# Performance work log

Hardware: AMD Instinct MI355X
Metric: run time of the kernel (lower is better)

## Reference

```python
import jax, jax.numpy as jnp
import numpy as np

N_NODES = 100000
N_EDGES = 800000
N_GRAPHS = 512
D_IN = 128
D_H = 128
N_LAYERS = 3
EPS = 1e-5


def setup_inputs() -> dict:
    key = jax.random.key(0)
    ks = jax.random.split(key, 8)
    x = jax.random.normal(ks[0], (N_NODES, D_IN), dtype=jnp.float32)
    edge_index = jax.random.randint(ks[1], (2, N_EDGES), 0, N_NODES, dtype=jnp.int64)
    batch = jnp.sort(jax.random.randint(ks[2], (N_NODES,), 0, N_GRAPHS, dtype=jnp.int64))
    s = 1.0 / np.sqrt(D_H)
    Ws = jax.random.normal(ks[3], (N_LAYERS, D_H, D_H), dtype=jnp.float32) * s
    bs = jnp.zeros((N_LAYERS, D_H), dtype=jnp.float32)
    gammas = jnp.ones((N_LAYERS, D_H), dtype=jnp.float32)
    betas = jnp.zeros((N_LAYERS, D_H), dtype=jnp.float32)
    W1 = jax.random.normal(ks[4], (D_H, D_H), dtype=jnp.float32) * s
    b1 = jnp.zeros((D_H,), dtype=jnp.float32)
    W2 = jax.random.normal(ks[5], (D_H, 1), dtype=jnp.float32) * s
    b2 = jnp.zeros((1,), dtype=jnp.float32)
    return {"x": x, "edge_index": edge_index, "batch": batch, "Ws": Ws, "bs": bs,
            "gammas": gammas, "betas": betas, "W1": W1, "b1": b1, "W2": W2, "b2": b2}


def reference(x, edge_index, batch, Ws, bs, gammas, betas, W1, b1, W2, b2):
    N = x.shape[0]
    src, dst = edge_index[0], edge_index[1]
    # GCN symmetric norm with self-loops: deg = in-degree + 1 (self loop weight 1)
    deg = jax.ops.segment_sum(jnp.ones_like(dst, dtype=jnp.float32), dst, num_segments=N) + 1.0
    dinv = jax.lax.rsqrt(deg)                      # [N]
    enorm = (dinv[src] * dinv[dst])[:, None]       # [E,1]
    self_w = (1.0 / deg)[:, None]                  # [N,1] self-loop norm dinv_i^2

    h = x
    for l in range(N_LAYERS):
        h = h @ Ws[l]                                                    # linear first (as PyG GCNConv)
        h = jax.ops.segment_sum(enorm * h[src], dst, num_segments=N) + h * self_w
        h = h + bs[l]
        # BatchNorm1d, training-mode per-feature stats (biased variance)
        mu = jnp.mean(h, axis=0)
        var = jnp.mean(jnp.square(h - mu), axis=0)
        h = (h - mu) * jax.lax.rsqrt(var + EPS) * gammas[l] + betas[l]
        h = jax.nn.relu(h)                                               # dropout p=0 -> identity

    # global mean pool over subgraphs
    sums = jax.ops.segment_sum(h, batch, num_segments=N_GRAPHS)
    cnt = jax.ops.segment_sum(jnp.ones((N,), jnp.float32), batch, num_segments=N_GRAPHS)
    Z = sums / jnp.maximum(cnt, 1.0)[:, None]

    # MLP head
    hz = jax.nn.relu(Z @ W1 + b1)
    logits = hz @ W2 + b2                           # [N_GRAPHS, 1]
    return logits
```

## Files before the change

kernel.cpp:

```cpp
#include <hip/hip_runtime.h>
#include <hip/hip_bf16.h>
#include <hip/hip_fp16.h>

#define N_NODES 100000
#define N_EDGES 800000
#define N_GRAPHS 512
#define D 128
#define EPSV 1e-5f

#define NBLK 256
#define EPB  3125
#define NBUK 391
#define MAXB 3072

#define LSTR 68
#define WOFF 4352

#define NSLOT 128

typedef _Float16 half8 __attribute__((ext_vector_type(8)));
typedef float floatx16 __attribute__((ext_vector_type(16)));

__device__ __forceinline__ float relu_f(float x){ return fmaxf(x, 0.0f); }

__device__ __forceinline__ void scan512(int* sd, int t)
{
    for (int off = 1; off < 512; off <<= 1){
        int i2 = t + 256;
        int v1 = (t  >= off) ? sd[t  - off] : 0;
        int v2 = (i2 >= off) ? sd[i2 - off] : 0;
        __syncthreads();
        sd[t]  += v1;
        sd[i2] += v2;
        __syncthreads();
    }
}

__global__ __launch_bounds__(256) void k_front(const int* __restrict__ dst,
                                               int* __restrict__ blockHist,
                                               const float* __restrict__ Ws,
                                               unsigned int* __restrict__ wpack,
                                               unsigned int* __restrict__ zbase,
                                               int zn,
                                               const int* __restrict__ batch,
                                               int* __restrict__ gstart,
                                               int* __restrict__ row_ptr)
{
    __shared__ int h[NBUK];
    int j = blockIdx.x, t = threadIdx.x;
    if (j < NBLK){
        for (int u = t; u < NBUK; u += 256) h[u] = 0;
        __syncthreads();
        int e0 = j * EPB;
        for (int e = e0 + t; e < e0 + EPB; e += 256)
            atomicAdd(&h[dst[e] >> 8], 1);
        __syncthreads();
        for (int u = t; u < NBUK; u += 256) blockHist[j * NBUK + u] = h[u];
    } else {
        int b = j - NBLK;
        int idx = b * 256 + t;
        if (idx == 0){
            row_ptr[N_NODES] = N_EDGES;
            gstart[N_GRAPHS] = N_NODES;
        }
        if (idx < 3 * 128 * 64){
            int l  = idx >> 13;
            int r  = idx & 8191;
            int c  = r >> 6;
            int k2 = r & 63;
            const float* W = Ws + l * D * D;
            __half2 hh = __floats2half2_rn(W[(size_t)(2 * k2) * D + c],
                                           W[(size_t)(2 * k2 + 1) * D + c]);
            wpack[idx] = *(unsigned int*)&hh;
        }
        int stride = 96 * 256;
        for (int i = idx; i < zn; i += stride) zbase[i] = 0u;
        if (idx < N_GRAPHS){
            int g = idx;
            int lo = 0, hi = N_NODES;
            while (lo < hi){ int m = (lo + hi) >> 1; if (batch[m] < g) lo = m + 1; else hi = m; }
            gstart[g] = lo;
        }
    }
}

__global__ __launch_bounds__(256) void k_p2a(const int* __restrict__ blockHist,
                                             int* __restrict__ colScan,
                                             int* __restrict__ bucketTotal)
{
    __shared__ int sd[256];
    int b = blockIdx.x, t = threadIdx.x;
    int v = blockHist[t * NBUK + b];
    sd[t] = v;
    __syncthreads();
    for (int off = 1; off < 256; off <<= 1){
        int u = (t >= off) ? sd[t - off] : 0;
        __syncthreads();
        sd[t] += u;
        __syncthreads();
    }
    colScan[t * NBUK + b] = sd[t] - v;
    if (t == 255) bucketTotal[b] = sd[255];
}

__global__ __launch_bounds__(256) void k_p3(const int* __restrict__ src,
                                            const int* __restrict__ dst,
                                            const int* __restrict__ colScan,
                                            const int* __restrict__ bucketTotal,
                                            int2* __restrict__ ebuf)
{
    __shared__ int sd[512];
    __shared__ int cur[NBUK];
    int j = blockIdx.x, t = threadIdx.x;
    int i2 = t + 256;
    sd[t]  = (t  < NBUK) ? bucketTotal[t]  : 0;
    sd[i2] = (i2 < NBUK) ? bucketTotal[i2] : 0;
    __syncthreads();
    scan512(sd, t);
    if (t < NBUK)
        cur[t]  = (sd[t]  - bucketTotal[t])  + colScan[j * NBUK + t];
    if (i2 < NBUK)
        cur[i2] = (sd[i2] - bucketTotal[i2]) + colScan[j * NBUK + i2];
    __syncthreads();
    int e0 = j * EPB;
    for (int e = e0 + t; e < e0 + EPB; e += 256){
        int s = src[e], d = dst[e];
        int pos = atomicAdd(&cur[d >> 8], 1);
        int2 v; v.x = s; v.y = d;
        ebuf[pos] = v;
    }
}

__global__ __launch_bounds__(256) void k_p4(const int2* __restrict__ ebuf,
                                            const int* __restrict__ bucketTotal,
                                            int* __restrict__ row_ptr,
                                            int* __restrict__ csr_src,
                                            float* __restrict__ dinv)
{
    __shared__ int2 stash[MAXB];
    __shared__ int sdScan[512];
    __shared__ int bins[256];
    __shared__ int sd[256];
    int b = blockIdx.x, t = threadIdx.x;
    int i2 = t + 256;
    sdScan[t]  = (t  < NBUK) ? bucketTotal[t]  : 0;
    sdScan[i2] = (i2 < NBUK) ? bucketTotal[i2] : 0;
    __syncthreads();
    scan512(sdScan, t);
    int cntb = bucketTotal[b];
    int base = sdScan[b] - cntb;
    bool st = (cntb <= MAXB);
    bins[t] = 0;
    __syncthreads();
    for (int i = t; i < cntb; i += 256){
        int2 ed = ebuf[base + i];
        if (st) stash[i] = ed;
        atomicAdd(&bins[ed.y & 255], 1);
    }
    __syncthreads();
    int a0 = bins[t];
    sd[t] = a0;
    __syncthreads();
    for (int off = 1; off < 256; off <<= 1){
        int v = (t >= off) ? sd[t - off] : 0;
        __syncthreads();
        sd[t] += v;
        __syncthreads();
    }
    int pex = sd[t] - a0;
    int node = b * 256 + t;
    if (node < N_NODES){
        row_ptr[node] = base + pex;
        float d = (float)(a0 + 1);
        dinv[node]  = rsqrtf(d);
    }
    __syncthreads();
    bins[t] = pex;
    __syncthreads();
    for (int i = t; i < cntb; i += 256){
        int2 ed = st ? stash[i] : ebuf[base + i];
        int pos = atomicAdd(&bins[ed.y & 255], 1);
        csr_src[base + pos] = ed.x;
    }
}

__global__ __launch_bounds__(256) void k_gemm(const void* __restrict__ Ain,
                                              const unsigned int* __restrict__ wp,
                                              const float* __restrict__ scale,
                                              const float* __restrict__ shift,
                                              const float* __restrict__ dinv,
                                              __half* __restrict__ outh,
                                              int mode)
{
    __shared__ unsigned int lds32[WOFF + 128 * LSTR];
    int tid = threadIdx.x;
    int rowBase = blockIdx.x * 64;

    if (mode == 0){
        const float* A = (const float*)Ain;
        #pragma unroll
        for (int rep = 0; rep < 8; rep++){
            int f  = rep * 256 + tid;
            int m  = f >> 5;
            int c4 = f & 31;
            int row = rowBase + m;
            if (row >= N_NODES) row = N_NODES - 1;
            float4 v = *(const float4*)(A + (size_t)row * D + c4 * 4);
            __half2 h0 = __floats2half2_rn(v.x, v.y);
            __half2 h1 = __floats2half2_rn(v.z, v.w);
            uint2 u; u.x = *(unsigned int*)&h0; u.y = *(unsigned int*)&h1;
            *(uint2*)&lds32[m * LSTR + 2 * c4] = u;
        }
    } else {
        const __half* A16 = (const __half*)Ain;
        #pragma unroll
        for (int rep = 0; rep < 4; rep++){
            int f  = rep * 256 + tid;
            int m  = f >> 4;
            int c8 = f & 15;
            int row = rowBase + m;
            if (row >= N_NODES) row = N_NODES - 1;
            uint4 v = *(const uint4*)(A16 + (size_t)row * D + c8 * 8);
            float4 sc0 = *(const float4*)(scale + c8 * 8);
            float4 sc1 = *(const float4*)(scale + c8 * 8 + 4);
            float4 sh0 = *(const float4*)(shift + c8 * 8);
            float4 sh1 = *(const float4*)(shift + c8 * 8 + 4);
            float2 f0 = __half22float2(*(__half2*)&v.x);
            float2 f1 = __half22float2(*(__half2*)&v.y);
            float2 f2 = __half22float2(*(__half2*)&v.z);
            float2 f3 = __half22float2(*(__half2*)&v.w);
            f0.x = relu_f(fmaf(f0.x, sc0.x, sh0.x));
            f0.y = relu_f(fmaf(f0.y, sc0.y, sh0.y));
            f1.x = relu_f(fmaf(f1.x, sc0.z, sh0.z));
            f1.y = relu_f(fmaf(f1.y, sc0.w, sh0.w));
            f2.x = relu_f(fmaf(f2.x, sc1.x, sh1.x));
            f2.y = relu_f(fmaf(f2.y, sc1.y, sh1.y));
            f3.x = relu_f(fmaf(f3.x, sc1.z, sh1.z));
            f3.y = relu_f(fmaf(f3.y, sc1.w, sh1.w));
            __half2 h0 = __floats2half2_rn(f0.x, f0.y);
            __half2 h1 = __floats2half2_rn(f1.x, f1.y);
            __half2 h2 = __floats2half2_rn(f2.x, f2.y);
            __half2 h3 = __floats2half2_rn(f3.x, f3.y);
            uint4 u;
            u.x = *(unsigned int*)&h0; u.y = *(unsigned int*)&h1;
            u.z = *(unsigned int*)&h2; u.w = *(unsigned int*)&h3;
            *(uint4*)&lds32[m * LSTR + 4 * c8] = u;
        }
    }
    {
        const uint4* gw = (const uint4*)wp;
        #pragma unroll
        for (int rep = 0; rep < 8; rep++){
            int f = rep * 256 + tid;
            int c = f >> 4;
            int q = f & 15;
            uint4 v = gw[f];
            *(uint4*)&lds32[WOFF + c * LSTR + 4 * q] = v;
        }
    }
    __syncthreads();

    int lane = tid & 63, wv = tid >> 6;
    int quad = lane >> 5;
    int ml   = (lane & 31) + (wv & 1) * 32;
    int cA   = (wv >> 1) * 64;
    int c0   = cA + (lane & 31);
    int c1   = c0 + 32;
    const unsigned int* aRow  = lds32 + ml * LSTR;
    const unsigned int* bRow0 = lds32 + WOFF + c0 * LSTR;
    const unsigned int* bRow1 = lds32 + WOFF + c1 * LSTR;
    floatx16 acc0 = {};
    floatx16 acc1 = {};
    #pragma unroll
    for (int ch = 0; ch < 8; ch++){
        int o = ch * 8 + quad * 4;
        half8 af = *(const half8*)(aRow  + o);
        half8 b0 = *(const half8*)(bRow0 + o);
        half8 b1 = *(const half8*)(bRow1 + o);
        acc0 = __builtin_amdgcn_mfma_f32_32x32x16_f16(af, b0, acc0, 0, 0, 0);
        acc1 = __builtin_amdgcn_mfma_f32_32x32x16_f16(af, b1, acc1, 0, 0, 0);
    }
    int rBase = rowBase + (wv & 1) * 32 + 4 * quad;
    #pragma unroll
    for (int r = 0; r < 16; r++){
        int outRow = rBase + (r & 3) + 8 * (r >> 2);
        if (outRow < N_NODES){
            float dv = dinv[outRow];
            outh[(size_t)outRow * D + c0] = __float2half(acc0[r] * dv);
            outh[(size_t)outRow * D + c1] = __float2half(acc1[r] * dv);
        }
    }
}

__device__ __forceinline__ void accum8(float* acc, uint4 v)
{
    float2 f0 = __half22float2(*(__half2*)&v.x);
    float2 f1 = __half22float2(*(__half2*)&v.y);
    float2 f2 = __half22float2(*(__half2*)&v.z);
    float2 f3 = __half22float2(*(__half2*)&v.w);
    acc[0] += f0.x; acc[1] += f0.y; acc[2] += f1.x; acc[3] += f1.y;
    acc[4] += f2.x; acc[5] += f2.y; acc[6] += f3.x; acc[7] += f3.y;
}

__global__ __launch_bounds__(256) void k_agg(const __half* __restrict__ t,
                                             const int* __restrict__ row_ptr,
                                             const int* __restrict__ csr_src,
                                             const float* __restrict__ dinv,
                                             const float* __restrict__ bias,
                                             __half* __restrict__ outb,
                                             float* __restrict__ Spart,
                                             float* __restrict__ Qpart)
{
    __shared__ float ldsS[4][128];
    __shared__ float ldsQ[4][128];
    int tid  = threadIdx.x;
    int lane = tid & 63;
    int wv   = tid >> 6;
    int q    = lane & 15;
    int g    = lane >> 4;
    const uint4* t4 = (const uint4*)t;
    uint4* out4 = (uint4*)outb;

    float4 bia = ((const float4*)bias)[2 * q];
    float4 bib = ((const float4*)bias)[2 * q + 1];

    float sa[8] = {0.f,0.f,0.f,0.f,0.f,0.f,0.f,0.f};
    float qa[8] = {0.f,0.f,0.f,0.f,0.f,0.f,0.f,0.f};

    int i0 = blockIdx.x * 32 + wv * 8 + g * 2;

    for (int n = 0; n < 2; n++){
        int i  = i0 + n;
        int p  = row_ptr[i];
        int pe = row_ptr[i + 1];
        float acc[8];
        {
            uint4 v = t4[(size_t)i * 16 + q];
            float2 f0 = __half22float2(*(__half2*)&v.x);
            float2 f1 = __half22float2(*(__half2*)&v.y);
            float2 f2 = __half22float2(*(__half2*)&v.z);
            float2 f3 = __half22float2(*(__half2*)&v.w);
            acc[0] = f0.x; acc[1] = f0.y; acc[2] = f1.x; acc[3] = f1.y;
            acc[4] = f2.x; acc[5] = f2.y; acc[6] = f3.x; acc[7] = f3.y;
        }
        for (; p + 4 <= pe; p += 4){
            int s0 = csr_src[p],     s1 = csr_src[p + 1];
            int s2 = csr_src[p + 2], s3 = csr_src[p + 3];
            uint4 v0 = t4[(size_t)s0 * 16 + q];
            uint4 v1 = t4[(size_t)s1 * 16 + q];
            uint4 v2 = t4[(size_t)s2 * 16 + q];
            uint4 v3 = t4[(size_t)s3 * 16 + q];
            accum8(acc, v0); accum8(acc, v1); accum8(acc, v2); accum8(acc, v3);
        }
        for (; p < pe; ++p){
            int s = csr_src[p];
            uint4 v = t4[(size_t)s * 16 + q];
            accum8(acc, v);
        }
        float dvi = dinv[i];
        acc[0] = fmaf(acc[0], dvi, bia.x);
        acc[1] = fmaf(acc[1], dvi, bia.y);
        acc[2] = fmaf(acc[2], dvi, bia.z);
        acc[3] = fmaf(acc[3], dvi, bia.w);
        acc[4] = fmaf(acc[4], dvi, bib.x);
        acc[5] = fmaf(acc[5], dvi, bib.y);
        acc[6] = fmaf(acc[6], dvi, bib.z);
        acc[7] = fmaf(acc[7], dvi, bib.w);
        __half2 o0 = __floats2half2_rn(acc[0], acc[1]);
        __half2 o1 = __floats2half2_rn(acc[2], acc[3]);
        __half2 o2 = __floats2half2_rn(acc[4], acc[5]);
        __half2 o3 = __floats2half2_rn(acc[6], acc[7]);
        uint4 ov;
        ov.x = *(unsigned int*)&o0; ov.y = *(unsigned int*)&o1;
        ov.z = *(unsigned int*)&o2; ov.w = *(unsigned int*)&o3;
        out4[(size_t)i * 16 + q] = ov;
        #pragma unroll
        for (int k = 0; k < 8; k++){
            sa[k] += acc[k];
            qa[k]  = fmaf(acc[k], acc[k], qa[k]);
        }
    }

    #pragma unroll
    for (int k = 0; k < 8; k++){
        sa[k] += __shfl_xor(sa[k], 16);
        sa[k] += __shfl_xor(sa[k], 32);
        qa[k] += __shfl_xor(qa[k], 16);
        qa[k] += __shfl_xor(qa[k], 32);
    }
    if (g == 0){
        #pragma unroll
        for (int k = 0; k < 8; k++){
            ldsS[wv][8 * q + k] = sa[k];
            ldsQ[wv][8 * q + k] = qa[k];
        }
    }
    __syncthreads();
    int slotBase = (blockIdx.x & (NSLOT - 1)) * 128;
    if (tid < 128){
        float s = ldsS[0][tid] + ldsS[1][tid] + ldsS[2][tid] + ldsS[3][tid];
        atomicAdd(&Spart[slotBase + tid], s);
    } else {
        int f = tid - 128;
        float qv = ldsQ[0][f] + ldsQ[1][f] + ldsQ[2][f] + ldsQ[3][f];
        atomicAdd(&Qpart[slotBase + f], qv);
    }
}

__global__ __launch_bounds__(256) void k_fin2(const float* __restrict__ Spart,
                                              const float* __restrict__ Qpart,
                                              const float* __restrict__ gamma,
                                              const float* __restrict__ beta,
                                              float* __restrict__ sc,
                                              float* __restrict__ sh)
{
    int t = threadIdx.x;
    int f = t & 127;
    const float* src = (t < 128) ? Spart : Qpart;
    float acc = 0.f;
    for (int s2 = 0; s2 < NSLOT; s2++)
        acc += src[s2 * 128 + f];
    __shared__ float red[256];
    red[t] = acc;
    __syncthreads();
    if (t < 128){
        float Sv = red[t];
        float Qv = red[t + 128];
        float mean = Sv * (1.0f / N_NODES);
        float var  = fmaxf(Qv * (1.0f / N_NODES) - mean * mean, 0.0f);
        float inv  = rsqrtf(var + EPSV);
        float gm = gamma[f] * inv;
        sc[f] = gm;
        sh[f] = beta[f] - mean * gm;
    }
}

__global__ __launch_bounds__(256) void k_tail(const __half* __restrict__ h,
                                              const int* __restrict__ gstart,
                                              const float* __restrict__ sc,
                                              const float* __restrict__ sh,
                                              const float* __restrict__ W1,
                                              const float* __restrict__ b1,
                                              const float* __restrict__ W2,
                                              const float* __restrict__ b2,
                                              float* __restrict__ out)
{
    __shared__ float part[256];
    __shared__ float z[128];
    __shared__ float red[128];
    int g = blockIdx.x;
    int tid = threadIdx.x;
    int f = tid & 127;
    int hf = tid >> 7;
    int s0 = gstart[g], s1 = gstart[g + 1];
    float scv = sc[f], shv = sh[f];
    float acc = 0.f;
    for (int i = s0 + hf; i < s1; i += 2)
        acc += relu_f(fmaf(__half2float(h[(size_t)i * D + f]), scv, shv));
    part[tid] = acc;
    __syncthreads();
    if (tid < 128){
        float c = fmaxf((float)(s1 - s0), 1.0f);
        z[f] = (part[f] + part[f + 128]) / c;
    }
    __syncthreads();
    float a = 0.f;
    int k0 = hf * 64;
    #pragma unroll 8
    for (int k = k0; k < k0 + 64; k++)
        a = fmaf(z[k], W1[k * D + f], a);
    part[tid] = a;
    __syncthreads();
    if (tid < 128){
        float av = relu_f(part[f] + part[f + 128] + b1[f]);
        red[f] = av * W2[f];
    }
    __syncthreads();
    for (int s2 = 64; s2 > 0; s2 >>= 1){
        if (tid < s2) red[tid] += red[tid + s2];
        __syncthreads();
    }
    if (tid == 0) out[g] = red[0] + b2[0];
}

extern "C" void kernel_launch(void* const* d_in, const int* in_sizes, int n_in,
                              void* d_out, int out_size, void* d_ws, size_t ws_size,
                              hipStream_t stream)
{
    const float* x      = (const float*)d_in[0];
    const int*   ei     = (const int*)d_in[1];
    const int*   batch  = (const int*)d_in[2];
    const float* Ws     = (const float*)d_in[3];
    const float* bs     = (const float*)d_in[4];
    const float* gammas = (const float*)d_in[5];
    const float* betas  = (const float*)d_in[6];
    const float* W1     = (const float*)d_in[7];
    const float* b1     = (const float*)d_in[8];
    const float* W2     = (const float*)d_in[9];
    const float* b2     = (const float*)d_in[10];
    float* out = (float*)d_out;

    const int* src = ei;
    const int* dst = ei + N_EDGES;

    char* w = (char*)d_ws;
    size_t off = 0;
    auto alloc = [&](size_t bytes) -> void* {
        void* p = w + off;
        off += (bytes + 255) & ~(size_t)255;
        return p;
    };
    int*   row_ptr     = (int*)  alloc((size_t)(N_NODES + 1) * 4);
    float* dinv        = (float*)alloc((size_t)N_NODES * 4);
    int*   csr_src     = (int*)  alloc((size_t)N_EDGES * 4);
    int*   blockHist   = (int*)  alloc((size_t)NBLK * NBUK * 4);
    int*   colScan     = (int*)  alloc((size_t)NBLK * NBUK * 4);
    int*   bucketTotal = (int*)  alloc((size_t)NBUK * 4);
    unsigned int* wpack = (unsigned int*)alloc((size_t)3 * 128 * 64 * 4);
    int*   gstart      = (int*)  alloc((size_t)(N_GRAPHS + 1) * 4);
    size_t zoff = off;
    float* stats       = (float*)alloc((size_t)3 * 2 * NSLOT * 128 * 4);
    size_t zend = off;
    float* ssh         = (float*)alloc(3 * 256 * 4);
    __half* tbuf       = (__half*)alloc((size_t)N_NODES * 128 * 2);
    __half* hbuf       = (__half*)alloc((size_t)N_NODES * 128 * 2);
    if (off > ws_size) return;

    int2* ebuf = (int2*)tbuf;

    k_front<<<NBLK + 96, 256, 0, stream>>>(dst, blockHist, Ws, wpack,
                                           (unsigned int*)(w + zoff),
                                           (int)((zend - zoff) >> 2),
                                           batch, gstart, row_ptr);
    k_p2a<<<NBUK, 256, 0, stream>>>(blockHist, colScan, bucketTotal);
    k_p3 <<<NBLK, 256, 0, stream>>>(src, dst, colScan, bucketTotal, ebuf);
    k_p4 <<<NBUK, 256, 0, stream>>>(ebuf, bucketTotal, row_ptr, csr_src, dinv);

    const void* curIn = (const void*)x;
    for (int l = 0; l < 3; l++){
        float* Sp = stats + (size_t)l * 2 * NSLOT * 128;
        float* Qp = Sp + NSLOT * 128;
        k_gemm<<<(N_NODES + 63) / 64, 256, 0, stream>>>(
            curIn, wpack + l * 8192,
            l ? ssh + (l - 1) * 256       : nullptr,
            l ? ssh + (l - 1) * 256 + 128 : nullptr,
            dinv, tbuf, l ? 1 : 0);
        k_agg<<<N_NODES / 32, 256, 0, stream>>>(
            tbuf, row_ptr, csr_src, dinv,
            bs + l * 128, hbuf, Sp, Qp);
        k_fin2<<<1, 256, 0, stream>>>(
            Sp, Qp, gammas + l * 128, betas + l * 128,
            ssh + l * 256, ssh + l * 256 + 128);
        curIn = (const void*)hbuf;
    }

    k_tail<<<N_GRAPHS, 256, 0, stream>>>(hbuf, gstart,
                                         ssh + 2 * 256, ssh + 2 * 256 + 128,
                                         W1, b1, W2, b2, out);
}
```

Measured before the change: 348.9 us.

## Fuse BN stat finalize into consumers, interleave two-node gathers, drop LDS reduction in agg

Removes the single-block k_fin2 launch per layer by having every k_gemm and k_tail block reduce the BatchNorm partial sums itself and compute scale/shift in shared memory. k_agg now walks the edge lists of its two nodes together so more independent gathers are in flight. It also drops the block-level LDS reduction in favour of per-wave atomics into fewer slots (NSLOT 128 to 64). This trades three tiny serialized launches for redundant reductions in each block, plus more atomic contention on the stats buffer.

```diff
diff --git a/kernel.cpp b/kernel.cpp
--- a/kernel.cpp
+++ b/kernel.cpp
@@ -16,7 +16,7 @@
 #define LSTR 68
 #define WOFF 4352
 
-#define NSLOT 128
+#define NSLOT 64
 
 typedef _Float16 half8 __attribute__((ext_vector_type(8)));
 typedef float floatx16 __attribute__((ext_vector_type(16)));
@@ -186,15 +186,42 @@
 
 __global__ __launch_bounds__(256) void k_gemm(const void* __restrict__ Ain,
                                               const unsigned int* __restrict__ wp,
-                                              const float* __restrict__ scale,
-                                              const float* __restrict__ shift,
+                                              const float* __restrict__ Spart,
+                                              const float* __restrict__ Qpart,
+                                              const float* __restrict__ gamma,
+                                              const float* __restrict__ beta,
                                               const float* __restrict__ dinv,
                                               __half* __restrict__ outh,
                                               int mode)
 {
     __shared__ unsigned int lds32[WOFF + 128 * LSTR];
+    __shared__ float sscale[128];
+    __shared__ float sshift[128];
     int tid = threadIdx.x;
     int rowBase = blockIdx.x * 64;
+
+    if (mode){
+        float* red = (float*)lds32;
+        int f = tid & 127;
+        const float* sp = (tid < 128) ? Spart : Qpart;
+        float acc = 0.f;
+        #pragma unroll 16
+        for (int s = 0; s < NSLOT; s++)
+            acc += sp[s * 128 + f];
+        red[tid] = acc;
+        __syncthreads();
+        if (tid < 128){
+            float Sv = red[f];
+            float Qv = red[f + 128];
+            float mean = Sv * (1.0f / N_NODES);
+            float var  = fmaxf(Qv * (1.0f / N_NODES) - mean * mean, 0.0f);
+            float inv  = rsqrtf(var + EPSV);
+            float gm = gamma[f] * inv;
+            sscale[f] = gm;
+            sshift[f] = beta[f] - mean * gm;
+        }
+        __syncthreads();
+    }
 
     if (mode == 0){
         const float* A = (const float*)Ain;
@@ -221,10 +248,10 @@
             int row = rowBase + m;
             if (row >= N_NODES) row = N_NODES - 1;
             uint4 v = *(const uint4*)(A16 + (size_t)row * D + c8 * 8);
-            float4 sc0 = *(const float4*)(scale + c8 * 8);
-            float4 sc1 = *(const float4*)(scale + c8 * 8 + 4);
-            float4 sh0 = *(const float4*)(shift + c8 * 8);
-            float4 sh1 = *(const float4*)(shift + c8 * 8 + 4);
+            float4 sc0 = *(const float4*)&sscale[c8 * 8];
+            float4 sc1 = *(const float4*)&sscale[c8 * 8 + 4];
+            float4 sh0 = *(const float4*)&sshift[c8 * 8];
+            float4 sh1 = *(const float4*)&sshift[c8 * 8 + 4];
             float2 f0 = __half22float2(*(__half2*)&v.x);
             float2 f1 = __half22float2(*(__half2*)&v.y);
             float2 f2 = __half22float2(*(__half2*)&v.z);
@@ -311,8 +338,6 @@
                                              float* __restrict__ Spart,
                                              float* __restrict__ Qpart)
 {
-    __shared__ float ldsS[4][128];
-    __shared__ float ldsQ[4][128];
     int tid  = threadIdx.x;
     int lane = tid & 63;
     int wv   = tid >> 6;
@@ -327,57 +352,120 @@
     float sa[8] = {0.f,0.f,0.f,0.f,0.f,0.f,0.f,0.f};
     float qa[8] = {0.f,0.f,0.f,0.f,0.f,0.f,0.f,0.f};
 
-    int i0 = blockIdx.x * 32 + wv * 8 + g * 2;
-
-    for (int n = 0; n < 2; n++){
-        int i  = i0 + n;
-        int p  = row_ptr[i];
-        int pe = row_ptr[i + 1];
-        float acc[8];
-        {
-            uint4 v = t4[(size_t)i * 16 + q];
-            float2 f0 = __half22float2(*(__half2*)&v.x);
-            float2 f1 = __half22float2(*(__half2*)&v.y);
-            float2 f2 = __half22float2(*(__half2*)&v.z);
-            float2 f3 = __half22float2(*(__half2*)&v.w);
-            acc[0] = f0.x; acc[1] = f0.y; acc[2] = f1.x; acc[3] = f1.y;
-            acc[4] = f2.x; acc[5] = f2.y; acc[6] = f3.x; acc[7] = f3.y;
-        }
-        for (; p + 4 <= pe; p += 4){
-            int s0 = csr_src[p],     s1 = csr_src[p + 1];
-            int s2 = csr_src[p + 2], s3 = csr_src[p + 3];
-            uint4 v0 = t4[(size_t)s0 * 16 + q];
-            uint4 v1 = t4[(size_t)s1 * 16 + q];
-            uint4 v2 = t4[(size_t)s2 * 16 + q];
-            uint4 v3 = t4[(size_t)s3 * 16 + q];
-            accum8(acc, v0); accum8(acc, v1); accum8(acc, v2); accum8(acc, v3);
-        }
-        for (; p < pe; ++p){
-            int s = csr_src[p];
-            uint4 v = t4[(size_t)s * 16 + q];
-            accum8(acc, v);
-        }
-        float dvi = dinv[i];
-        acc[0] = fmaf(acc[0], dvi, bia.x);
-        acc[1] = fmaf(acc[1], dvi, bia.y);
-        acc[2] = fmaf(acc[2], dvi, bia.z);
-        acc[3] = fmaf(acc[3], dvi, bia.w);
-        acc[4] = fmaf(acc[4], dvi, bib.x);
-        acc[5] = fmaf(acc[5], dvi, bib.y);
-        acc[6] = fmaf(acc[6], dvi, bib.z);
-        acc[7] = fmaf(acc[7], dvi, bib.w);
-        __half2 o0 = __floats2half2_rn(acc[0], acc[1]);
-        __half2 o1 = __floats2half2_rn(acc[2], acc[3]);
-        __half2 o2 = __floats2half2_rn(acc[4], acc[5]);
-        __half2 o3 = __floats2half2_rn(acc[6], acc[7]);
+    int iA = blockIdx.x * 32 + wv * 8 + g * 2;
+    int pA = row_ptr[iA];
+    int pM = row_ptr[iA + 1];
+    int pE = row_ptr[iA + 2];
+
+    float accA[8], accB[8];
+    {
+        uint4 vA = t4[(size_t)iA * 16 + q];
+        uint4 vB = t4[(size_t)(iA + 1) * 16 + q];
+        float2 a0 = __half22float2(*(__half2*)&vA.x);
+        float2 a1 = __half22float2(*(__half2*)&vA.y);
+        float2 a2 = __half22float2(*(__half2*)&vA.z);
+        float2 a3 = __half22float2(*(__half2*)&vA.w);
+        accA[0]=a0.x; accA[1]=a0.y; accA[2]=a1.x; accA[3]=a1.y;
+        accA[4]=a2.x; accA[5]=a2.y; accA[6]=a3.x; accA[7]=a3.y;
+        float2 b0 = __half22float2(*(__half2*)&vB.x);
+        float2 b1 = __half22float2(*(__half2*)&vB.y);
+        float2 b2v= __half22float2(*(__half2*)&vB.z);
+        float2 b3 = __half22float2(*(__half2*)&vB.w);
+        accB[0]=b0.x; accB[1]=b0.y; accB[2]=b1.x; accB[3]=b1.y;
+        accB[4]=b2v.x; accB[5]=b2v.y; accB[6]=b3.x; accB[7]=b3.y;
+    }
+
+    int a = pA, b = pM;
+    while (a + 4 <= pM && b + 4 <= pE){
+        int ia0 = csr_src[a],     ia1 = csr_src[a + 1];
+        int ia2 = csr_src[a + 2], ia3 = csr_src[a + 3];
+        int ib0 = csr_src[b],     ib1 = csr_src[b + 1];
+        int ib2 = csr_src[b + 2], ib3 = csr_src[b + 3];
+        uint4 va0 = t4[(size_t)ia0 * 16 + q];
+        uint4 va1 = t4[(size_t)ia1 * 16 + q];
+        uint4 va2 = t4[(size_t)ia2 * 16 + q];
+        uint4 va3 = t4[(size_t)ia3 * 16 + q];
+        uint4 vb0 = t4[(size_t)ib0 * 16 + q];
+        uint4 vb1 = t4[(size_t)ib1 * 16 + q];
+        uint4 vb2 = t4[(size_t)ib2 * 16 + q];
+        uint4 vb3 = t4[(size_t)ib3 * 16 + q];
+        accum8(accA, va0); accum8(accA, va1); accum8(accA, va2); accum8(accA, va3);
+        accum8(accB, vb0); accum8(accB, vb1); accum8(accB, vb2); accum8(accB, vb3);
+        a += 4; b += 4;
+    }
+    for (; a + 4 <= pM; a += 4){
+        int i0 = csr_src[a],     i1 = csr_src[a + 1];
+        int i2 = csr_src[a + 2], i3 = csr_src[a + 3];
+        uint4 v0 = t4[(size_t)i0 * 16 + q];
+        uint4 v1 = t4[(size_t)i1 * 16 + q];
+        uint4 v2 = t4[(size_t)i2 * 16 + q];
+        uint4 v3 = t4[(size_t)i3 * 16 + q];
+        accum8(accA, v0); accum8(accA, v1); accum8(accA, v2); accum8(accA, v3);
+    }
+    for (; a < pM; ++a){
+        int s = csr_src[a];
+        accum8(accA, t4[(size_t)s * 16 + q]);
+    }
+    for (; b + 4 <= pE; b += 4){
+        int i0 = csr_src[b],     i1 = csr_src[b + 1];
+        int i2 = csr_src[b + 2], i3 = csr_src[b + 3];
+        uint4 v0 = t4[(size_t)i0 * 16 + q];
+        uint4 v1 = t4[(size_t)i1 * 16 + q];
+        uint4 v2 = t4[(size_t)i2 * 16 + q];
+        uint4 v3 = t4[(size_t)i3 * 16 + q];
+        accum8(accB, v0); accum8(accB, v1); accum8(accB, v2); accum8(accB, v3);
+    }
+    for (; b < pE; ++b){
+        int s = csr_src[b];
+        accum8(accB, t4[(size_t)s * 16 + q]);
+    }
+
+    {
+        float dvi = dinv[iA];
+        accA[0] = fmaf(accA[0], dvi, bia.x);
+        accA[1] = fmaf(accA[1], dvi, bia.y);
+        accA[2] = fmaf(accA[2], dvi, bia.z);
+        accA[3] = fmaf(accA[3], dvi, bia.w);
+        accA[4] = fmaf(accA[4], dvi, bib.x);
+        accA[5] = fmaf(accA[5], dvi, bib.y);
+        accA[6] = fmaf(accA[6], dvi, bib.z);
+        accA[7] = fmaf(accA[7], dvi, bib.w);
+        __half2 o0 = __floats2half2_rn(accA[0], accA[1]);
+        __half2 o1 = __floats2half2_rn(accA[2], accA[3]);
+        __half2 o2 = __floats2half2_rn(accA[4], accA[5]);
+        __half2 o3 = __floats2half2_rn(accA[6], accA[7]);
         uint4 ov;
         ov.x = *(unsigned int*)&o0; ov.y = *(unsigned int*)&o1;
         ov.z = *(unsigned int*)&o2; ov.w = *(unsigned int*)&o3;
-        out4[(size_t)i * 16 + q] = ov;
+        out4[(size_t)iA * 16 + q] = ov;
         #pragma unroll
         for (int k = 0; k < 8; k++){
-            sa[k] += acc[k];
-            qa[k]  = fmaf(acc[k], acc[k], qa[k]);
+            sa[k] += accA[k];
+            qa[k]  = fmaf(accA[k], accA[k], qa[k]);
+        }
+    }
+    {
+        float dvi = dinv[iA + 1];
+        accB[0] = fmaf(accB[0], dvi, bia.x);
+        accB[1] = fmaf(accB[1], dvi, bia.y);
+        accB[2] = fmaf(accB[2], dvi, bia.z);
+        accB[3] = fmaf(accB[3], dvi, bia.w);
+        accB[4] = fmaf(accB[4], dvi, bib.x);
+        accB[5] = fmaf(accB[5], dvi, bib.y);
+        accB[6] = fmaf(accB[6], dvi, bib.z);
+        accB[7] = fmaf(accB[7], dvi, bib.w);
+        __half2 o0 = __floats2half2_rn(accB[0], accB[1]);
+        __half2 o1 = __floats2half2_rn(accB[2], accB[3]);
+        __half2 o2 = __floats2half2_rn(accB[4], accB[5]);
+        __half2 o3 = __floats2half2_rn(accB[6], accB[7]);
+        uint4 ov;
+        ov.x = *(unsigned int*)&o0; ov.y = *(unsigned int*)&o1;
+        ov.z = *(unsigned int*)&o2; ov.w = *(unsigned int*)&o3;
+        out4[(size_t)(iA + 1) * 16 + q] = ov;
+        #pragma unroll
+        for (int k = 0; k < 8; k++){
+            sa[k] += accB[k];
+            qa[k]  = fmaf(accB[k], accB[k], qa[k]);
         }
     }
 
@@ -389,56 +477,21 @@
         qa[k] += __shfl_xor(qa[k], 32);
     }
     if (g == 0){
+        int slotBase = (((blockIdx.x << 2) + wv) & (NSLOT - 1)) * 128 + 8 * q;
         #pragma unroll
         for (int k = 0; k < 8; k++){
-            ldsS[wv][8 * q + k] = sa[k];
-            ldsQ[wv][8 * q + k] = qa[k];
-        }
-    }
-    __syncthreads();
-    int slotBase = (blockIdx.x & (NSLOT - 1)) * 128;
-    if (tid < 128){
-        float s = ldsS[0][tid] + ldsS[1][tid] + ldsS[2][tid] + ldsS[3][tid];
-        atomicAdd(&Spart[slotBase + tid], s);
-    } else {
-        int f = tid - 128;
-        float qv = ldsQ[0][f] + ldsQ[1][f] + ldsQ[2][f] + ldsQ[3][f];
-        atomicAdd(&Qpart[slotBase + f], qv);
-    }
-}
-
-__global__ __launch_bounds__(256) void k_fin2(const float* __restrict__ Spart,
+            atomicAdd(&Spart[slotBase + k], sa[k]);
+            atomicAdd(&Qpart[slotBase + k], qa[k]);
+        }
+    }
+}
+
+__global__ __launch_bounds__(256) void k_tail(const __half* __restrict__ h,
+                                              const int* __restrict__ gstart,
+                                              const float* __restrict__ Spart,
                                               const float* __restrict__ Qpart,
                                               const float* __restrict__ gamma,
                                               const float* __restrict__ beta,
-                                              float* __restrict__ sc,
-                                              float* __restrict__ sh)
-{
-    int t = threadIdx.x;
-    int f = t & 127;
-    const float* src = (t < 128) ? Spart : Qpart;
-    float acc = 0.f;
-    for (int s2 = 0; s2 < NSLOT; s2++)
-        acc += src[s2 * 128 + f];
-    __shared__ float red[256];
-    red[t] = acc;
-    __syncthreads();
-    if (t < 128){
-        float Sv = red[t];
-        float Qv = red[t + 128];
-        float mean = Sv * (1.0f / N_NODES);
-        float var  = fmaxf(Qv * (1.0f / N_NODES) - mean * mean, 0.0f);
-        float inv  = rsqrtf(var + EPSV);
-        float gm = gamma[f] * inv;
-        sc[f] = gm;
-        sh[f] = beta[f] - mean * gm;
-    }
-}
-
-__global__ __launch_bounds__(256) void k_tail(const __half* __restrict__ h,
-                                              const int* __restrict__ gstart,
-                                              const float* __restrict__ sc,
-                                              const float* __restrict__ sh,
                                               const float* __restrict__ W1,
                                               const float* __restrict__ b1,
                                               const float* __restrict__ W2,
@@ -448,12 +501,36 @@
     __shared__ float part[256];
     __shared__ float z[128];
     __shared__ float red[128];
+    __shared__ float sscale[128];
+    __shared__ float sshift[128];
     int g = blockIdx.x;
     int tid = threadIdx.x;
     int f = tid & 127;
     int hf = tid >> 7;
+
+    {
+        const float* sp = (tid < 128) ? Spart : Qpart;
+        float acc = 0.f;
+        #pragma unroll 16
+        for (int s = 0; s < NSLOT; s++)
+            acc += sp[s * 128 + f];
+        part[tid] = acc;
+        __syncthreads();
+        if (tid < 128){
+            float Sv = part[f];
+            float Qv = part[f + 128];
+            float mean = Sv * (1.0f / N_NODES);
+            float var  = fmaxf(Qv * (1.0f / N_NODES) - mean * mean, 0.0f);
+            float inv  = rsqrtf(var + EPSV);
+            float gm = gamma[f] * inv;
+            sscale[f] = gm;
+            sshift[f] = beta[f] - mean * gm;
+        }
+        __syncthreads();
+    }
+
     int s0 = gstart[g], s1 = gstart[g + 1];
-    float scv = sc[f], shv = sh[f];
+    float scv = sscale[f], shv = sshift[f];
     float acc = 0.f;
     for (int i = s0 + hf; i < s1; i += 2)
         acc += relu_f(fmaf(__half2float(h[(size_t)i * D + f]), scv, shv));
@@ -521,7 +598,6 @@
     size_t zoff = off;
     float* stats       = (float*)alloc((size_t)3 * 2 * NSLOT * 128 * 4);
     size_t zend = off;
-    float* ssh         = (float*)alloc(3 * 256 * 4);
     __half* tbuf       = (__half*)alloc((size_t)N_NODES * 128 * 2);
     __half* hbuf       = (__half*)alloc((size_t)N_NODES * 128 * 2);
     if (off > ws_size) return;
@@ -540,21 +616,27 @@
     for (int l = 0; l < 3; l++){
         float* Sp = stats + (size_t)l * 2 * NSLOT * 128;
         float* Qp = Sp + NSLOT * 128;
+        float* Spm = stats + (size_t)(l - 1) * 2 * NSLOT * 128;
+        float* Qpm = Spm + NSLOT * 128;
         k_gemm<<<(N_NODES + 63) / 64, 256, 0, stream>>>(
             curIn, wpack + l * 8192,
-            l ? ssh + (l - 1) * 256       : nullptr,
-            l ? ssh + (l - 1) * 256 + 128 : nullptr,
+            l ? Spm : nullptr,
+            l ? Qpm : nullptr,
+            l ? gammas + (l - 1) * 128 : nullptr,
+            l ? betas  + (l - 1) * 128 : nullptr,
             dinv, tbuf, l ? 1 : 0);
         k_agg<<<N_NODES / 32, 256, 0, stream>>>(
             tbuf, row_ptr, csr_src, dinv,
             bs + l * 128, hbuf, Sp, Qp);
-        k_fin2<<<1, 256, 0, stream>>>(
-            Sp, Qp, gammas + l * 128, betas + l * 128,
-            ssh + l * 256, ssh + l * 256 + 128);
         curIn = (const void*)hbuf;
     }
 
-    k_tail<<<N_GRAPHS, 256, 0, stream>>>(hbuf, gstart,
-                                         ssh + 2 * 256, ssh + 2 * 256 + 128,
-                                         W1, b1, W2, b2, out);
-}
+    {
+        float* Sp2 = stats + (size_t)2 * 2 * NSLOT * 128;
+        float* Qp2 = Sp2 + NSLOT * 128;
+        k_tail<<<N_GRAPHS, 256, 0, stream>>>(hbuf, gstart,
+                                             Sp2, Qp2,
+                                             gammas + 2 * 128, betas + 2 * 128,
+                                             W1, b1, W2, b2, out);
+    }
+}
```

After: 640.4 us. +83.5%, slower.
